# Optimization experiments

Hardware: AMD Instinct MI355X
Metric: run time of the kernel (lower is better)

## Reference

```python
import jax, jax.numpy as jnp
import numpy as np

ALPHA = 100.0  # self.softmax_alpha


def _interp_nearest(x, size):
    # torch F.interpolate mode='nearest': src_idx = floor(dst_idx * H_in / H_out)
    H, W = x.shape[-2], x.shape[-1]
    h, w = size
    ri = (jnp.arange(h) * H) // h
    ci = (jnp.arange(w) * W) // w
    return x[:, :, ri, :][:, :, :, ci]


def _interp_bilinear_ac(x, size):
    # torch F.interpolate mode='bilinear', align_corners=True
    H, W = x.shape[-2], x.shape[-1]
    h, w = size

    def coords(n_out, n_in):
        if n_out == 1:
            return jnp.zeros((1,), jnp.float32)
        return jnp.arange(n_out, dtype=jnp.float32) * ((n_in - 1) / (n_out - 1))

    ry, rx = coords(h, H), coords(w, W)
    y0 = jnp.floor(ry).astype(jnp.int32)
    x0 = jnp.floor(rx).astype(jnp.int32)
    y1 = jnp.clip(y0 + 1, 0, H - 1)
    x1 = jnp.clip(x0 + 1, 0, W - 1)
    wy = (ry - y0.astype(jnp.float32))[None, None, :, None]
    wx = (rx - x0.astype(jnp.float32))[None, None, None, :]
    rows = x[:, :, y0, :] * (1.0 - wy) + x[:, :, y1, :] * wy  # (n,c,h,W)
    return rows[:, :, :, x0] * (1.0 - wx) + rows[:, :, :, x1] * wx  # (n,c,h,w)


def _warp(unalign_fb, fa, fa_parse, fb, fb_parse, alpha):
    n, c, h, w = fa.shape
    c2 = unalign_fb.shape[1]
    hw = h * w
    # center and channel-normalize features per spatial location
    fa = fa - jnp.mean(fa, axis=(2, 3), keepdims=True)
    fb = fb - jnp.mean(fb, axis=(2, 3), keepdims=True)
    fa = fa.reshape(n, c, hw)
    fb = fb.reshape(n, c, hw)
    fa = fa / jnp.linalg.norm(fa, axis=1, keepdims=True)
    fb = fb / jnp.linalg.norm(fb, axis=1, keepdims=True)
    ufb = unalign_fb.reshape(n, c2, hw)
    mask_a = (fa_parse.reshape(n, -1, hw)[:, 1:, :] != 0).astype(fa.dtype)  # (n,K,hw)
    mask_b = (fb_parse.reshape(n, -1, hw)[:, 1:, :] != 0).astype(fb.dtype)
    local_fa = fa[:, None, :, :] * mask_a[:, :, None, :]  # (n,K,c,hw)
    local_fb = fb[:, None, :, :] * mask_b[:, :, None, :]  # (n,K,c,hw)
    # energy[n,k,q,p] = sum_c local_fb[n,k,c,q] * local_fa[n,k,c,p]
    energy = jnp.einsum('nkcq,nkcp->nkqp', local_fb, local_fa) * alpha
    corr = jax.nn.softmax(energy, axis=2)  # softmax over fb locations q
    warped = jnp.einsum('ncq,nkqp->nkcp', ufb, corr)  # (n,K,c2,hw)
    combined = (warped * mask_a[:, :, None, :]).sum(axis=1)  # (n,c2,hw)
    norm = jnp.maximum(mask_a.sum(axis=1, keepdims=True), 1.0)  # (n,1,hw)
    aligned = combined / norm
    return aligned.reshape(n, c2, h, w)


def setup_inputs() -> dict:
    key = jax.random.key(0)
    k1, k2, k3, k4, k5 = jax.random.split(key, 5)
    return {
        'unalign_fb': jax.random.normal(k1, (1, 64, 256, 256), jnp.float32),
        'fa': jax.random.normal(k2, (1, 256, 64, 64), jnp.float32),
        'fa_parse': jax.random.randint(k3, (1, 4, 256, 256), 0, 2).astype(jnp.int32),
        'fb': jax.random.normal(k4, (1, 256, 64, 64), jnp.float32),
        'fb_parse': jax.random.randint(k5, (1, 4, 256, 256), 0, 2).astype(jnp.int32),
    }


def reference(unalign_fb, fa, fa_parse, fb, fb_parse):
    raw_hw = unalign_fb.shape[-2:]
    feat_hw = fa.shape[-2:]
    fa_p = _interp_nearest(fa_parse, feat_hw)
    fb_p = _interp_nearest(fb_parse, feat_hw)
    ufb = _interp_bilinear_ac(unalign_fb, fb.shape[-2:])
    aligned = _warp(ufb, fa, fa_p, fb, fb_p, ALPHA)
    return _interp_bilinear_ac(aligned, raw_hw)
```

## Files before the change

### kernel.cpp

```cpp
#include <hip/hip_runtime.h>
#include <math.h>

#define HW 4096
#define CC 256
#define C2 64
#define E50f 1.928749848e-22f

typedef unsigned short USH;
typedef __attribute__((ext_vector_type(8))) _Float16 f16x8;
typedef __attribute__((ext_vector_type(8))) short bf8;
typedef __attribute__((ext_vector_type(4))) float f32x4;

__device__ __forceinline__ USH f2bf(float x) {
    unsigned u = __float_as_uint(x);
    u += 0x7fff + ((u >> 16) & 1);
    return (USH)(u >> 16);
}
__device__ __forceinline__ USH f2h(float x) {
    _Float16 h = (_Float16)x;
    return *(USH*)&h;
}

__device__ __forceinline__ void gl2lds16(const USH* g, USH* l) {
    __builtin_amdgcn_global_load_lds(
        (const __attribute__((address_space(1))) void*)g,
        (__attribute__((address_space(3))) void*)l, 16, 0, 0);
}

__global__ void k_prep1(const float* __restrict__ fa, const float* __restrict__ fb,
                        float* __restrict__ mu,
                        const float* __restrict__ ufb_src, const int* __restrict__ fb_parse,
                        USH* __restrict__ vtT, float* __restrict__ bgp) {
    __shared__ float4 sred[256];
    int t = threadIdx.x;
    if (blockIdx.x < 512) {
        int b = blockIdx.x;
        const float* src = (b < CC) ? (fa + b * HW) : (fb + (b - CC) * HW);
        float s = 0.f;
        for (int q = t; q < HW; q += 256) s += src[q];
        sred[t].x = s;
        __syncthreads();
        for (int st = 128; st > 0; st >>= 1) {
            if (t < st) sred[t].x += sred[t + st].x;
            __syncthreads();
        }
        if (t == 0) mu[b] = sred[0].x * (1.0f / HW);
        return;
    }
    int bid = blockIdx.x - 512;
    int pblk = bid & 15, c = bid >> 4;
    int p = pblk * 256 + t;
    int j = p >> 6, i = p & 63;
    int off = (4 * j) * 256 + 4 * i;
    float m0 = (fb_parse[1 * 65536 + off] != 0) ? 1.f : 0.f;
    float m1 = (fb_parse[2 * 65536 + off] != 0) ? 1.f : 0.f;
    float m2 = (fb_parse[3 * 65536 + off] != 0) ? 1.f : 0.f;
    float ry = j * (255.0f / 63.0f);
    int y0 = (int)ry; y0 = min(y0, 255); int y1 = min(y0 + 1, 255);
    float wy = ry - (float)y0;
    float rx = i * (255.0f / 63.0f);
    int x0 = (int)rx; x0 = min(x0, 255); int x1 = min(x0 + 1, 255);
    float wx = rx - (float)x0;
    const float* sc = ufb_src + c * 65536;
    float r0 = sc[y0 * 256 + x0] * (1.f - wx) + sc[y0 * 256 + x1] * wx;
    float r1 = sc[y1 * 256 + x0] * (1.f - wx) + sc[y1 * 256 + x1] * wx;
    float v = r0 * (1.f - wy) + r1 * wy;
    size_t cbase = (size_t)(p >> 5) * 8192 + (p & 31);
    vtT[cbase + (0 * 65 + c) * 32] = f2bf(v * m0);
    vtT[cbase + (1 * 65 + c) * 32] = f2bf(v * m1);
    vtT[cbase + (2 * 65 + c) * 32] = f2bf(v * m2);
    if (c == 0) {
        vtT[cbase + 64 * 32]  = f2bf(m0);
        vtT[cbase + 129 * 32] = f2bf(m1);
        vtT[cbase + 194 * 32] = f2bf(m2);
        for (int m = 195; m < 256; ++m) vtT[cbase + m * 32] = 0;
    }
    sred[t] = make_float4(v, v * m0, v * m1, v * m2);
    __syncthreads();
    for (int st = 128; st > 0; st >>= 1) {
        if (t < st) {
            float4 o = sred[t + st];
            sred[t].x += o.x; sred[t].y += o.y; sred[t].z += o.z; sred[t].w += o.w;
        }
        __syncthreads();
    }
    if (t == 0) {
        float4 r = sred[0];
        bgp[pblk * 320 + 256 + c]     = r.x;
        bgp[pblk * 320 + 0 * 65 + c]  = r.y;
        bgp[pblk * 320 + 1 * 65 + c]  = r.z;
        bgp[pblk * 320 + 2 * 65 + c]  = r.w;
    }
    __syncthreads();
    if (c == 0) {
        sred[t] = make_float4(m0, m1, m2, 0.f);
        __syncthreads();
        for (int st = 128; st > 0; st >>= 1) {
            if (t < st) {
                float4 o = sred[t + st];
                sred[t].x += o.x; sred[t].y += o.y; sred[t].z += o.z;
            }
            __syncthreads();
        }
        if (t == 0) {
            float4 r = sred[0];
            bgp[pblk * 320 + 64]  = r.x;
            bgp[pblk * 320 + 129] = r.y;
            bgp[pblk * 320 + 194] = r.z;
        }
    }
}

__global__ __launch_bounds__(256) void k_normT(
    const float* __restrict__ fa, const float* __restrict__ fb,
    const float* __restrict__ mu_,
    USH* __restrict__ faT, USH* __restrict__ fbT) {
    __shared__ float tile[256][33];
    __shared__ float red[8][32];
    __shared__ float rv[32];
    int which = blockIdx.z;
    const float* src = which ? fb : fa;
    USH* dst = which ? fbT : faT;
    const float* mu = mu_ + which * CC;
    int p0 = blockIdx.x * 32;
    int t = threadIdx.x;
    int pi = t & 31, g = t >> 5;
    for (int it = 0; it < 32; ++it) {
        int c = it * 8 + g;
        tile[c][pi] = src[(size_t)c * HW + p0 + pi];
    }
    __syncthreads();
    float ss = 0.f;
#pragma unroll
    for (int jc = 0; jc < 32; ++jc) {
        float v = tile[g * 32 + jc][pi] - mu[g * 32 + jc];
        ss += v * v;
    }
    red[g][pi] = ss;
    __syncthreads();
    if (g == 0) {
        float s2 = 0.f;
#pragma unroll
        for (int gg = 0; gg < 8; ++gg) s2 += red[gg][pi];
        rv[pi] = rsqrtf(s2);
    }
    __syncthreads();
    float rinv = rv[pi];
    size_t base = (size_t)g * 131072 + (size_t)(p0 + pi) * 32;
#pragma unroll
    for (int seg = 0; seg < 4; ++seg) {
        union { USH us[8]; uint4 v; } h;
#pragma unroll
        for (int jc = 0; jc < 8; ++jc)
            h.us[jc] = f2h((tile[g * 32 + seg * 8 + jc][pi] - mu[g * 32 + seg * 8 + jc]) * rinv);
        *(uint4*)&dst[base + seg * 8] = h.v;
    }
}

__global__ __launch_bounds__(256, 2) void k_attn(
    const USH* __restrict__ faT, const USH* __restrict__ fbT,
    const USH* __restrict__ vtT, float* __restrict__ part) {
    __shared__ USH sA[8 * 2048];
    __shared__ USH sE[64 * 136];
    int t = threadIdx.x;
    int bid = blockIdx.x;
    int z = bid & 7;
    int p0 = (bid >> 3) * 64;
    int w = t >> 6, lane = t & 63, lr = lane & 15, quad = lane >> 4;
    f32x4 accp[4][4] = {};

#pragma unroll
    for (int kk = 0; kk < 2; ++kk) {
        int kc = 2 * w + kk;
#pragma unroll
        for (int seg = 0; seg < 4; ++seg)
            gl2lds16(faT + (size_t)kc * 131072 + (size_t)p0 * 32 + seg * 512 + lane * 8,
                     &sA[kc * 2048 + seg * 512]);
    }

    const USH* pB = fbT + (size_t)(z * 512 + 32 * w + lr) * 32 + quad * 8;
    const USH* pV = vtT + (size_t)(64 * w + lr) * 32 + quad * 8;

    __syncthreads();

    for (int qt = 0; qt < 4; ++qt) {
        f32x4 accs[2][4] = {};
#pragma unroll
        for (int kc = 0; kc < 8; ++kc) {
            f16x8 a[2], b[4];
#pragma unroll
            for (int i = 0; i < 2; ++i)
                a[i] = *(const f16x8*)&pB[(size_t)kc * 131072 + qt * 4096 + i * 512];
#pragma unroll
            for (int jj = 0; jj < 4; ++jj)
                b[jj] = *(const f16x8*)&sA[kc * 2048 + (16 * jj + lr) * 32 + quad * 8];
#pragma unroll
            for (int i = 0; i < 2; ++i)
#pragma unroll
                for (int jj = 0; jj < 4; ++jj)
                    accs[i][jj] = __builtin_amdgcn_mfma_f32_16x16x32_f16(a[i], b[jj], accs[i][jj], 0, 0, 0);
        }
        if (qt) __syncthreads();
#pragma unroll
        for (int i = 0; i < 2; ++i)
#pragma unroll
            for (int jj = 0; jj < 4; ++jj) {
                unsigned u0 = ((unsigned)f2bf(__expf(fmaf(100.f, accs[i][jj][1], -50.f))) << 16)
                            | (unsigned)f2bf(__expf(fmaf(100.f, accs[i][jj][0], -50.f)));
                unsigned u1 = ((unsigned)f2bf(__expf(fmaf(100.f, accs[i][jj][3], -50.f))) << 16)
                            | (unsigned)f2bf(__expf(fmaf(100.f, accs[i][jj][2], -50.f)));
                int addr = (16 * jj + lr) * 136 + 32 * w + 16 * i + 4 * quad;
                uint2 u; u.x = u0; u.y = u1;
                *(uint2*)&sE[addr] = u;
            }
        __syncthreads();
#pragma unroll
        for (int kc = 0; kc < 4; ++kc) {
            size_t vb = (size_t)(z * 16 + qt * 4 + kc) * 8192;
            bf8 av[4] = {}, be[4];
#pragma unroll
            for (int i = 0; i < 4; ++i)
                if (!(w == 3 && i > 0))
                    av[i] = *(const bf8*)&pV[vb + i * 512];
#pragma unroll
            for (int jj = 0; jj < 4; ++jj)
                be[jj] = *(const bf8*)&sE[(16 * jj + lr) * 136 + kc * 32 + quad * 8];
#pragma unroll
            for (int i = 0; i < 4; ++i)
#pragma unroll
                for (int jj = 0; jj < 4; ++jj)
                    if (!(w == 3 && i > 0))
                        accp[i][jj] = __builtin_amdgcn_mfma_f32_16x16x32_bf16(av[i], be[jj], accp[i][jj], 0, 0, 0);
        }
    }
    float* op = part + (size_t)z * 1048576;
#pragma unroll
    for (int i = 0; i < 4; ++i) {
        int m = 64 * w + 16 * i + quad * 4;
#pragma unroll
        for (int jj = 0; jj < 4; ++jj) {
            int pc = p0 + 16 * jj + lr;
#pragma unroll
            for (int r = 0; r < 4; ++r)
                if (m + r < 195)
                    op[(size_t)(m + r) * HW + pc] = accp[i][jj][r];
        }
    }
}

__global__ void k_combine8(const float* __restrict__ part, const float* __restrict__ bgp,
                           const int* __restrict__ fa_parse, float* __restrict__ aligned) {
    __shared__ float sden[3];
    __shared__ float sc2[4][4];
    int t = threadIdx.x;
    int cg = blockIdx.y * 4;
    if (t < 19) {
        int idx;
        if (t < 3) idx = t * 65 + 64;
        else {
            int lc = (t - 3) >> 2, r = (t - 3) & 3;
            idx = (r < 3) ? r * 65 + (cg + lc) : 256 + (cg + lc);
        }
        float s = 0.f;
#pragma unroll
        for (int pb = 0; pb < 16; ++pb) s += bgp[pb * 320 + idx];
        if (t < 3) sden[t] = s;
        else sc2[(t - 3) >> 2][(t - 3) & 3] = s;
    }
    __syncthreads();
    int p = blockIdx.x * 256 + t;
    int jj = p >> 6, ii = p & 63;
    int off = (4 * jj) * 256 + 4 * ii;
    float ma[3], den[3];
    float s = 0.f;
#pragma unroll
    for (int k = 0; k < 3; ++k) {
        ma[k] = (fa_parse[(k + 1) * 65536 + off] != 0) ? 1.f : 0.f;
        s += ma[k];
        den[k] = E50f * (4096.0f - sden[k]);
        size_t rd = (size_t)(k * 65 + 64) * HW + p;
#pragma unroll
        for (int z = 0; z < 8; ++z) den[k] += part[(size_t)z * 1048576 + rd];
    }
    float fs = fmaxf(s, 1.f);
#pragma unroll
    for (int lc = 0; lc < 4; ++lc) {
        int c2 = cg + lc;
        float num = 0.f;
#pragma unroll
        for (int k = 0; k < 3; ++k) {
            float nu = E50f * (sc2[lc][3] - sc2[lc][k]);
            size_t rn = (size_t)(k * 65 + c2) * HW + p;
#pragma unroll
            for (int z = 0; z < 8; ++z) nu += part[(size_t)z * 1048576 + rn];
            num += ma[k] * (nu / den[k]);
        }
        aligned[(size_t)c2 * HW + p] = num / fs;
    }
}

__global__ void k_bilin_up(const float* __restrict__ aligned, float* __restrict__ out) {
    int idx = (blockIdx.x * 256 + threadIdx.x) * 4;
    int c2 = blockIdx.y;
    int y = idx >> 8;
    float ry = y * (63.0f / 255.0f);
    int y0 = (int)ry; y0 = min(y0, 63); int y1 = min(y0 + 1, 63);
    float wy = ry - (float)y0;
    const float* a = aligned + c2 * HW;
    float4 o;
    float* op = &o.x;
#pragma unroll
    for (int u = 0; u < 4; ++u) {
        int x = (idx & 255) + u;
        float rx = x * (63.0f / 255.0f);
        int x0 = (int)rx; x0 = min(x0, 63); int x1 = min(x0 + 1, 63);
        float wx = rx - (float)x0;
        float r0 = a[y0 * 64 + x0] * (1.f - wx) + a[y0 * 64 + x1] * wx;
        float r1 = a[y1 * 64 + x0] * (1.f - wx) + a[y1 * 64 + x1] * wx;
        op[u] = r0 * (1.f - wy) + r1 * wy;
    }
    *(float4*)&out[c2 * 65536 + idx] = o;
}

extern "C" void kernel_launch(void* const* d_in, const int* in_sizes, int n_in,
                              void* d_out, int out_size, void* d_ws, size_t ws_size,
                              hipStream_t stream) {
    const float* unalign_fb = (const float*)d_in[0];
    const float* fa         = (const float*)d_in[1];
    const int*   fa_parse   = (const int*)d_in[2];
    const float* fb         = (const float*)d_in[3];
    const int*   fb_parse   = (const int*)d_in[4];
    float* out = (float*)d_out;

    float* w = (float*)d_ws;
    float* mu       = w;
    float* bgp      = w + 66048;
    float* part     = w + 71168;
    float* aligned  = w + 8459776;
    USH* faT = (USH*)(w + 8721920);
    USH* fbT = (USH*)(w + 9246208);
    USH* vtT = (USH*)(w + 9770496);

    k_prep1<<<dim3(1536), dim3(256), 0, stream>>>(fa, fb, mu, unalign_fb, fb_parse, vtT, bgp);
    k_normT<<<dim3(128, 1, 2), dim3(256), 0, stream>>>(fa, fb, mu, faT, fbT);
    k_attn<<<dim3(512), dim3(256), 0, stream>>>(faT, fbT, vtT, part);
    k_combine8<<<dim3(16, 16), dim3(256), 0, stream>>>(part, bgp, fa_parse, aligned);
    k_bilin_up<<<dim3(64, 64), dim3(256), 0, stream>>>(aligned, out);
}
```

Baseline: 130.2 us.

## Widen attention tile to 128 query columns with 8 waves per block

The attention kernel now processes 128 fa positions per block using 512 threads (8 waves) instead of 64 positions with 256 threads. Each wave loads one fb row fragment and reuses it across eight fa column tiles, and the PV stage splits the output channels across eight waves at 32 rows each. This halves the grid and raises reuse of the streamed fb and V tiles per block, at the cost of larger LDS (sA 64KB plus sE) and possibly lower occupancy, since two 512-thread blocks per CU may not fit.

```diff
diff --git a/kernel.cpp b/kernel.cpp
--- a/kernel.cpp
+++ b/kernel.cpp
@@ -157,88 +157,78 @@
     }
 }
 
-__global__ __launch_bounds__(256, 2) void k_attn(
+__global__ __launch_bounds__(512, 2) void k_attn(
     const USH* __restrict__ faT, const USH* __restrict__ fbT,
     const USH* __restrict__ vtT, float* __restrict__ part) {
-    __shared__ USH sA[8 * 2048];
-    __shared__ USH sE[64 * 136];
+    __shared__ USH sA[8 * 4096];
+    __shared__ USH sE[128 * 136];
     int t = threadIdx.x;
     int bid = blockIdx.x;
     int z = bid & 7;
-    int p0 = (bid >> 3) * 64;
+    int p0 = (bid >> 3) * 128;
     int w = t >> 6, lane = t & 63, lr = lane & 15, quad = lane >> 4;
-    f32x4 accp[4][4] = {};
-
-#pragma unroll
-    for (int kk = 0; kk < 2; ++kk) {
-        int kc = 2 * w + kk;
-#pragma unroll
-        for (int seg = 0; seg < 4; ++seg)
-            gl2lds16(faT + (size_t)kc * 131072 + (size_t)p0 * 32 + seg * 512 + lane * 8,
-                     &sA[kc * 2048 + seg * 512]);
-    }
-
-    const USH* pB = fbT + (size_t)(z * 512 + 32 * w + lr) * 32 + quad * 8;
-    const USH* pV = vtT + (size_t)(64 * w + lr) * 32 + quad * 8;
+    f32x4 accp[2][8] = {};
+
+#pragma unroll
+    for (int seg = 0; seg < 8; ++seg)
+        gl2lds16(faT + (size_t)w * 131072 + (size_t)p0 * 32 + seg * 512 + lane * 8,
+                 &sA[w * 4096 + seg * 512]);
+
+    const USH* pB = fbT + (size_t)(z * 512 + 16 * w + lr) * 32 + quad * 8;
+    const USH* pV = vtT + (size_t)(32 * w + lr) * 32 + quad * 8;
 
     __syncthreads();
 
     for (int qt = 0; qt < 4; ++qt) {
-        f32x4 accs[2][4] = {};
+        f32x4 accs[8] = {};
 #pragma unroll
         for (int kc = 0; kc < 8; ++kc) {
-            f16x8 a[2], b[4];
-#pragma unroll
-            for (int i = 0; i < 2; ++i)
-                a[i] = *(const f16x8*)&pB[(size_t)kc * 131072 + qt * 4096 + i * 512];
-#pragma unroll
-            for (int jj = 0; jj < 4; ++jj)
-                b[jj] = *(const f16x8*)&sA[kc * 2048 + (16 * jj + lr) * 32 + quad * 8];
-#pragma unroll
-            for (int i = 0; i < 2; ++i)
-#pragma unroll
-                for (int jj = 0; jj < 4; ++jj)
-                    accs[i][jj] = __builtin_amdgcn_mfma_f32_16x16x32_f16(a[i], b[jj], accs[i][jj], 0, 0, 0);
+            f16x8 a, b[8];
+            a = *(const f16x8*)&pB[(size_t)kc * 131072 + qt * 4096];
+#pragma unroll
+            for (int jj = 0; jj < 8; ++jj)
+                b[jj] = *(const f16x8*)&sA[kc * 4096 + (16 * jj + lr) * 32 + quad * 8];
+#pragma unroll
+            for (int jj = 0; jj < 8; ++jj)
+                accs[jj] = __builtin_amdgcn_mfma_f32_16x16x32_f16(a, b[jj], accs[jj], 0, 0, 0);
         }
         if (qt) __syncthreads();
 #pragma unroll
-        for (int i = 0; i < 2; ++i)
-#pragma unroll
-            for (int jj = 0; jj < 4; ++jj) {
-                unsigned u0 = ((unsigned)f2bf(__expf(fmaf(100.f, accs[i][jj][1], -50.f))) << 16)
-                            | (unsigned)f2bf(__expf(fmaf(100.f, accs[i][jj][0], -50.f)));
-                unsigned u1 = ((unsigned)f2bf(__expf(fmaf(100.f, accs[i][jj][3], -50.f))) << 16)
-                            | (unsigned)f2bf(__expf(fmaf(100.f, accs[i][jj][2], -50.f)));
-                int addr = (16 * jj + lr) * 136 + 32 * w + 16 * i + 4 * quad;
-                uint2 u; u.x = u0; u.y = u1;
-                *(uint2*)&sE[addr] = u;
-            }
+        for (int jj = 0; jj < 8; ++jj) {
+            unsigned u0 = ((unsigned)f2bf(__expf(fmaf(100.f, accs[jj][1], -50.f))) << 16)
+                        | (unsigned)f2bf(__expf(fmaf(100.f, accs[jj][0], -50.f)));
+            unsigned u1 = ((unsigned)f2bf(__expf(fmaf(100.f, accs[jj][3], -50.f))) << 16)
+                        | (unsigned)f2bf(__expf(fmaf(100.f, accs[jj][2], -50.f)));
+            int addr = (16 * jj + lr) * 136 + 16 * w + 4 * quad;
+            uint2 u; u.x = u0; u.y = u1;
+            *(uint2*)&sE[addr] = u;
+        }
         __syncthreads();
 #pragma unroll
         for (int kc = 0; kc < 4; ++kc) {
             size_t vb = (size_t)(z * 16 + qt * 4 + kc) * 8192;
-            bf8 av[4] = {}, be[4];
-#pragma unroll
-            for (int i = 0; i < 4; ++i)
-                if (!(w == 3 && i > 0))
+            bf8 av[2] = {}, be[8];
+#pragma unroll
+            for (int i = 0; i < 2; ++i)
+                if (!(w == 7 || (w == 6 && i == 1)))
                     av[i] = *(const bf8*)&pV[vb + i * 512];
 #pragma unroll
-            for (int jj = 0; jj < 4; ++jj)
+            for (int jj = 0; jj < 8; ++jj)
                 be[jj] = *(const bf8*)&sE[(16 * jj + lr) * 136 + kc * 32 + quad * 8];
 #pragma unroll
-            for (int i = 0; i < 4; ++i)
-#pragma unroll
-                for (int jj = 0; jj < 4; ++jj)
-                    if (!(w == 3 && i > 0))
+            for (int i = 0; i < 2; ++i)
+#pragma unroll
+                for (int jj = 0; jj < 8; ++jj)
+                    if (!(w == 7 || (w == 6 && i == 1)))
                         accp[i][jj] = __builtin_amdgcn_mfma_f32_16x16x32_bf16(av[i], be[jj], accp[i][jj], 0, 0, 0);
         }
     }
     float* op = part + (size_t)z * 1048576;
 #pragma unroll
-    for (int i = 0; i < 4; ++i) {
-        int m = 64 * w + 16 * i + quad * 4;
-#pragma unroll
-        for (int jj = 0; jj < 4; ++jj) {
+    for (int i = 0; i < 2; ++i) {
+        int m = 32 * w + 16 * i + 4 * quad;
+#pragma unroll
+        for (int jj = 0; jj < 8; ++jj) {
             int pc = p0 + 16 * jj + lr;
 #pragma unroll
             for (int r = 0; r < 4; ++r)
@@ -343,7 +333,7 @@
 
     k_prep1<<<dim3(1536), dim3(256), 0, stream>>>(fa, fb, mu, unalign_fb, fb_parse, vtT, bgp);
     k_normT<<<dim3(128, 1, 2), dim3(256), 0, stream>>>(fa, fb, mu, faT, fbT);
-    k_attn<<<dim3(512), dim3(256), 0, stream>>>(faT, fbT, vtT, part);
+    k_attn<<<dim3(256), dim3(512), 0, stream>>>(faT, fbT, vtT, part);
     k_combine8<<<dim3(16, 16), dim3(256), 0, stream>>>(part, bgp, fa_parse, aligned);
     k_bilin_up<<<dim3(64, 64), dim3(256), 0, stream>>>(aligned, out);
 }
```

Result: no change. 129.3 us (median of 2 runs) (-0.7%).
